# Kernel tuning notes

Measured on AMD Instinct MI355X. Metric: run time of the kernel, lower is better.

The kernel has to match this reference:

```python
import jax, jax.numpy as jnp
import numpy as np

N_NODES = 50000
N_EDGES = 800000
DIM = 256
HEADS = 8
DIM_OUT = 32  # per-head; dim_inner = HEADS*DIM_OUT = 256


def setup_inputs() -> dict:
    key = jax.random.key(0)
    ks = jax.random.split(key, 9)
    s = 1.0 / np.sqrt(DIM)
    inner = HEADS * DIM_OUT
    return {
        "x": jax.random.normal(ks[0], (N_NODES, DIM), dtype=jnp.float32),
        "Wq": jax.random.uniform(ks[1], (DIM, inner), jnp.float32, -s, s),
        "bq": jax.random.uniform(ks[2], (inner,), jnp.float32, -s, s),
        "Wk": jax.random.uniform(ks[3], (DIM, inner), jnp.float32, -s, s),
        "bk": jax.random.uniform(ks[4], (inner,), jnp.float32, -s, s),
        "Wv": jax.random.uniform(ks[5], (DIM, inner), jnp.float32, -s, s),
        "bv": jax.random.uniform(ks[6], (inner,), jnp.float32, -s, s),
        "src": jax.random.randint(ks[7], (N_EDGES,), 0, N_NODES),
        "dst": jax.random.randint(ks[8], (N_EDGES,), 0, N_NODES),
    }


def reference(x, Wq, bq, Wk, bk, Wv, bv, src, dst):
    n = x.shape[0]
    q = (x @ Wq + bq).reshape(n, HEADS, DIM_OUT)
    k = (x @ Wk + bk).reshape(n, HEADS, DIM_OUT)
    v = (x @ Wv + bv).reshape(n, HEADS, DIM_OUT)
    # edge-wise u_dot_v: dot of src query with dst key, per head -> [E, H]
    scores = jnp.einsum('ehd,ehd->eh', q[src], k[dst]) / jnp.sqrt(
        jnp.asarray(DIM_OUT, dtype=x.dtype))
    # segment softmax over incoming edges of each destination node
    m = jax.ops.segment_max(scores, dst, num_segments=n)  # [N, H]
    m = jnp.where(jnp.isfinite(m), m, 0.0)
    e = jnp.exp(scores - m[dst])
    z = jax.ops.segment_sum(e, dst, num_segments=n)  # [N, H]
    p = e / jnp.maximum(z[dst], 1e-16)  # [E, H]
    # u_mul_e_sum: sum over incoming edges of src values weighted by attn
    out = jax.ops.segment_sum(v[src] * p[:, :, None], dst, num_segments=n)
    return out.reshape(n, HEADS * DIM_OUT)  # concat=True
```

## Files before the change

### kernel.cpp

```cpp
#include <hip/hip_runtime.h>
#include <math.h>

#define N_NODES 50000
#define N_EDGES 800000
#define DIM 256
#define HEADS 8
#define DIM_OUT 32
#define INNER 256
#define M_PAD 50048

typedef __attribute__((ext_vector_type(8))) short bf16x8;
typedef __attribute__((ext_vector_type(4))) float f32x4;
typedef __attribute__((ext_vector_type(2))) float f32x2;

__device__ __forceinline__ unsigned short f2bf(float f) {
    unsigned u = __float_as_uint(f);
    unsigned r = (u + 0x7FFFu + ((u >> 16) & 1u)) >> 16;
    return (unsigned short)r;
}

__device__ __forceinline__ f32x2 up2(unsigned u) {
    f32x2 r;
    r.x = __uint_as_float(u << 16);
    r.y = __uint_as_float(u & 0xFFFF0000u);
    return r;
}
__device__ __forceinline__ void up2x4(uint4 r, f32x2* o) {
    o[0] = up2(r.x); o[1] = up2(r.y); o[2] = up2(r.z); o[3] = up2(r.w);
}

__device__ __forceinline__ void gll16(const void* g, void* l) {
    __builtin_amdgcn_global_load_lds(
        (const __attribute__((address_space(1))) unsigned*)(uintptr_t)g,
        (__attribute__((address_space(3))) unsigned*)(unsigned)(uintptr_t)l,
        16, 0, 0);
}

#define NB_CONVX 6256
#define NB_CONVW 768
#define NB_HIST  3125
__global__ __launch_bounds__(256) void prep(
    const float* __restrict__ x,
    const float* __restrict__ Wq, const float* __restrict__ Wk,
    const float* __restrict__ Wv,
    const int* __restrict__ dst,
    unsigned short* __restrict__ xbf, unsigned short* __restrict__ Wt,
    int* __restrict__ deg, int* __restrict__ rank)
{
    int b = blockIdx.x;
    if (b < NB_CONVX) {
        size_t i8 = ((size_t)b * 256 + threadIdx.x) * 8;
        unsigned short h[8];
        if (i8 < (size_t)N_NODES * 256) {
            float4 a = *(const float4*)(x + i8);
            float4 c = *(const float4*)(x + i8 + 4);
            h[0]=f2bf(a.x); h[1]=f2bf(a.y); h[2]=f2bf(a.z); h[3]=f2bf(a.w);
            h[4]=f2bf(c.x); h[5]=f2bf(c.y); h[6]=f2bf(c.z); h[7]=f2bf(c.w);
        } else {
            #pragma unroll
            for (int j = 0; j < 8; j++) h[j] = 0;
        }
        uint4 o;
        o.x = (unsigned)h[0] | ((unsigned)h[1] << 16);
        o.y = (unsigned)h[2] | ((unsigned)h[3] << 16);
        o.z = (unsigned)h[4] | ((unsigned)h[5] << 16);
        o.w = (unsigned)h[6] | ((unsigned)h[7] << 16);
        *(uint4*)(xbf + i8) = o;
    } else if (b < NB_CONVX + NB_CONVW) {
        int idx = (b - NB_CONVX) * 256 + threadIdx.x;
        int z = idx >> 16, r = idx & 65535;
        int k = r >> 8, n = r & 255;
        const float* W = (z == 0) ? Wq : (z == 1) ? Wk : Wv;
        Wt[(size_t)z * 65536 + n * 256 + k] = f2bf(W[k * 256 + n]);
    } else {
        int e = (b - NB_CONVX - NB_CONVW) * 256 + threadIdx.x;
        if (e < N_EDGES) rank[e] = atomicAdd(deg + dst[e], 1);
    }
}

#define GEMM_NWG 1173
__global__ __launch_bounds__(512) void gemm_qkv(
    const unsigned short* __restrict__ xbf,
    const unsigned short* __restrict__ Wt,
    const float* __restrict__ bq, const float* __restrict__ bk,
    const float* __restrict__ bv,
    unsigned short* __restrict__ q, unsigned short* __restrict__ k,
    unsigned short* __restrict__ v,
    const int* __restrict__ deg, int* __restrict__ rowptr)
{
    const int t = threadIdx.x;

    if (blockIdx.x == 0) {
        __shared__ int wsum[8];
        __shared__ int wpre[9];
        int wid = t >> 6, ln = t & 63;
        int carry = 0;
        for (int base = 0; base < N_NODES; base += 2048) {
            int i4 = base + t * 4;
            int4 dv = {0, 0, 0, 0};
            if (i4 < N_NODES) dv = *(const int4*)(deg + i4);
            int sum = dv.x + dv.y + dv.z + dv.w;
            int inc = sum;
            #pragma unroll
            for (int off = 1; off < 64; off <<= 1) {
                int u = __shfl_up(inc, off);
                if (ln >= off) inc += u;
            }
            if (ln == 63) wsum[wid] = inc;
            __syncthreads();
            if (t == 0) {
                int a = 0;
                #pragma unroll
                for (int j = 0; j < 8; j++) { wpre[j] = a; a += wsum[j]; }
                wpre[8] = a;
            }
            __syncthreads();
            if (i4 < N_NODES) {
                int r = carry + wpre[wid] + (inc - sum);
                r += dv.x; rowptr[i4 + 1] = r;
                r += dv.y; rowptr[i4 + 2] = r;
                r += dv.z; rowptr[i4 + 3] = r;
                r += dv.w; rowptr[i4 + 4] = r;
            }
            carry += wpre[8];
            __syncthreads();
        }
        if (t == 0) rowptr[0] = 0;
        return;
    }

    int hw = blockIdx.x - 1;
    int xcd = hw & 7, pos = hw >> 3;
    int lid = (xcd < 5 ? xcd * 147 : 5 * 147 + (xcd - 5) * 146) + pos;
    int panel = lid / 3;
    int z = lid - panel * 3;
    const int row0 = panel * 128;

    const unsigned short* Wz = Wt + (size_t)z * 65536;
    const float* bias = (z == 0) ? bq : (z == 1) ? bk : bv;
    unsigned short* C = (z == 0) ? q : (z == 1) ? k : v;

    __shared__ __align__(16) short As[2][128 * 32];
    __shared__ __align__(16) short Bs[2][256 * 32];

    const int wave = t >> 6;
    const int lane = t & 63;
    const int wm = (wave & 1) * 64;
    const int wn = (wave >> 1) * 64;
    const int lr = lane & 15;
    const int lg = lane >> 4;
    const int srow = lane >> 2;
    const int sch  = lane & 3;

    f32x4 acc[4][4] = {};

#define STAGE(B, K)                                                          \
    do {                                                                     \
        gll16(xbf + (size_t)(row0 + wave * 16 + srow) * 256 + (K) + sch * 8, \
              &As[B][wave * 512]);                                           \
        gll16(Wz + (size_t)(wave * 32 + srow) * 256 + (K) + sch * 8,         \
              &Bs[B][wave * 1024]);                                          \
        gll16(Wz + (size_t)(wave * 32 + 16 + srow) * 256 + (K) + sch * 8,    \
              &Bs[B][wave * 1024 + 512]);                                    \
    } while (0)

    STAGE(0, 0);
    #pragma unroll
    for (int s = 0; s < 8; s++) {
        const int cur = s & 1;
        __syncthreads();
        if (s < 7) STAGE(cur ^ 1, (s + 1) * 32);
        bf16x8 af[4], bfr[4];
        #pragma unroll
        for (int mi = 0; mi < 4; mi++)
            af[mi] = *(const bf16x8*)&As[cur][(wm + mi * 16 + lr) * 32 + lg * 8];
        #pragma unroll
        for (int ni = 0; ni < 4; ni++)
            bfr[ni] = *(const bf16x8*)&Bs[cur][(wn + ni * 16 + lr) * 32 + lg * 8];
        #pragma unroll
        for (int mi = 0; mi < 4; mi++)
            #pragma unroll
            for (int ni = 0; ni < 4; ni++)
                acc[mi][ni] = __builtin_amdgcn_mfma_f32_16x16x32_bf16(
                    af[mi], bfr[ni], acc[mi][ni], 0, 0, 0);
    }
#undef STAGE

    #pragma unroll
    for (int mi = 0; mi < 4; mi++) {
        #pragma unroll
        for (int ni = 0; ni < 4; ni++) {
            int gcol = wn + ni * 16 + lr;
            float bb = bias[gcol];
            #pragma unroll
            for (int r = 0; r < 4; r++) {
                int grow = row0 + wm + mi * 16 + lg * 4 + r;
                if (grow < N_NODES)
                    C[(size_t)grow * 256 + gcol] = f2bf(acc[mi][ni][r] + bb);
            }
        }
    }
}

__global__ __launch_bounds__(256) void csr_scatter(
    const int* __restrict__ src, const int* __restrict__ dst,
    const int* __restrict__ rowptr, const int* __restrict__ rank,
    int* __restrict__ edge_src)
{
    int e = blockIdx.x * 256 + threadIdx.x;
    if (e >= N_EDGES) return;
    edge_src[rowptr[dst[e]] + rank[e]] = src[e];
}

__global__ __launch_bounds__(256) void node_attn(
    const unsigned short* __restrict__ qbf,
    const unsigned short* __restrict__ kbf,
    const unsigned short* __restrict__ vbf,
    const int* __restrict__ rowptr, const int* __restrict__ edge_src,
    float* __restrict__ out)
{
    int node = blockIdx.x * 4 + (threadIdx.x >> 6);
    int lane = threadIdx.x & 63;
    if (node >= N_NODES) return;
    const int half = lane >> 5;
    const int l = lane & 31;

    int beg = rowptr[node], end = rowptr[node + 1];
    int deg = end - beg;

    float* op = out + (size_t)node * 256 + l * 8;
    if (deg <= 0) {
        if (half == 0) {
            float4 z4 = {0.f, 0.f, 0.f, 0.f};
            *(float4*)op = z4;
            *(float4*)(op + 4) = z4;
        }
        return;
    }

    f32x2 kf2[4];
    up2x4(*(const uint4*)(kbf + (size_t)node * 256 + l * 8), kf2);

    const unsigned short* qrow = qbf + l * 8;
    const unsigned short* vrow = vbf + l * 8;

    const float SC = 0.17677669529663687f * 1.4426950408889634f;

    int U = (deg + 1) >> 1;
    U = ((U + 2) / 3) * 3;
    U = __builtin_amdgcn_readfirstlane(U);

    const int i0 = beg + half;
    const int last = end - 1;

    int tmp0 = edge_src[min(i0,     last)];
    int tmp1 = edge_src[min(i0 + 2, last)];
    int idC  = edge_src[min(i0 + 4, last)];
    int idA  = edge_src[min(i0 + 6, last)];
    int idB  = 0;
    uint4 qA = *(const uint4*)(qrow + (size_t)tmp0 * 256);
    uint4 vA = *(const uint4*)(vrow + (size_t)tmp0 * 256);
    uint4 qB = *(const uint4*)(qrow + (size_t)tmp1 * 256);
    uint4 vB = *(const uint4*)(vrow + (size_t)tmp1 * 256);
    uint4 qC, vC;

    float m = -1e30f, zsum = 0.0f;
    f32x2 af2[4] = {};

#define BODY(QW, VW, QL, VL, IDL, IDF, P)                                    \
    do {                                                                     \
        size_t off_ = (size_t)(IDL) * 256;                                   \
        QL = *(const uint4*)(qrow + off_);                                   \
        VL = *(const uint4*)(vrow + off_);                                   \
        int vi_ = i0 + 2 * t + 2 * (P);                                      \
        IDF = edge_src[min(vi_ + 8, last)];                                  \
        f32x2 qf_[4], vf_[4];                                                \
        up2x4(QW, qf_);                                                      \
        up2x4(VW, vf_);                                                      \
        f32x2 d_ = qf_[0] * kf2[0];                                          \
        d_ += qf_[1] * kf2[1];                                               \
        d_ += qf_[2] * kf2[2];                                               \
        d_ += qf_[3] * kf2[3];                                               \
        float s_ = d_.x + d_.y;                                              \
        s_ += __shfl_xor(s_, 1);                                             \
        s_ += __shfl_xor(s_, 2);                                             \
        bool ok_ = vi_ < end;                                                \
        float sc_ = ok_ ? s_ * SC : -1e30f;                                  \
        float mn_ = fmaxf(m, sc_);                                           \
        float w_ = exp2f(sc_ - mn_);                                         \
        w_ = ok_ ? w_ : 0.0f;                                                \
        float al_ = exp2f(m - mn_);                                          \
        zsum = zsum * al_ + w_;                                              \
        f32x2 a2_ = {al_, al_}, w2_ = {w_, w_};                              \
        af2[0] = af2[0] * a2_ + vf_[0] * w2_;                                \
        af2[1] = af2[1] * a2_ + vf_[1] * w2_;                                \
        af2[2] = af2[2] * a2_ + vf_[2] * w2_;                                \
        af2[3] = af2[3] * a2_ + vf_[3] * w2_;                                \
        m = mn_;                                                             \
    } while (0)

    for (int t = 0; t < U; t += 3) {
        BODY(qA, vA, qC, vC, idC, idB, 0);
        BODY(qB, vB, qA, vA, idA, idC, 1);
        BODY(qC, vC, qB, vB, idB, idA, 2);
    }
#undef BODY

    float mo = __shfl_xor(m, 32);
    float mt = fmaxf(m, mo);
    float scale = exp2f(m - mt);
    zsum *= scale;
    zsum += __shfl_xor(zsum, 32);
    #pragma unroll
    for (int j = 0; j < 4; j++) {
        af2[j].x = af2[j].x * scale;
        af2[j].y = af2[j].y * scale;
        af2[j].x += __shfl_xor(af2[j].x, 32);
        af2[j].y += __shfl_xor(af2[j].y, 32);
    }

    float inv = 1.0f / fmaxf(zsum, 1e-16f);
    if (half == 0) {
        float4 o0 = {af2[0].x * inv, af2[0].y * inv, af2[1].x * inv, af2[1].y * inv};
        float4 o1 = {af2[2].x * inv, af2[2].y * inv, af2[3].x * inv, af2[3].y * inv};
        *(float4*)op = o0;
        *(float4*)(op + 4) = o1;
    }
}

extern "C" void kernel_launch(void* const* d_in, const int* in_sizes, int n_in,
                              void* d_out, int out_size, void* d_ws, size_t ws_size,
                              hipStream_t stream) {
    const float* x  = (const float*)d_in[0];
    const float* Wq = (const float*)d_in[1];
    const float* bq = (const float*)d_in[2];
    const float* Wk = (const float*)d_in[3];
    const float* bk = (const float*)d_in[4];
    const float* Wv = (const float*)d_in[5];
    const float* bv = (const float*)d_in[6];
    const int* src  = (const int*)d_in[7];
    const int* dst  = (const int*)d_in[8];
    float* out = (float*)d_out;

    unsigned short* qbf = (unsigned short*)d_ws;
    unsigned short* kbf = qbf + (size_t)N_NODES * INNER;
    unsigned short* vbf = kbf + (size_t)N_NODES * INNER;
    unsigned short* xbf = vbf + (size_t)N_NODES * INNER;
    unsigned short* Wt  = xbf + (size_t)M_PAD * INNER;
    int* deg      = (int*)(Wt + 3 * 65536);
    int* rowptr   = deg + N_NODES;
    int* edge_src = rowptr + (N_NODES + 1);
    int* rank     = edge_src + N_EDGES;

    hipMemsetAsync(deg, 0, (size_t)N_NODES * sizeof(int), stream);

    prep<<<NB_CONVX + NB_CONVW + NB_HIST, 256, 0, stream>>>(
        x, Wq, Wk, Wv, dst, xbf, Wt, deg, rank);

    gemm_qkv<<<GEMM_NWG + 1, 512, 0, stream>>>(
        xbf, Wt, bq, bk, bv, qbf, kbf, vbf, deg, rowptr);

    csr_scatter<<<(N_EDGES + 255) / 256, 256, 0, stream>>>(
        src, dst, rowptr, rank, edge_src);

    node_attn<<<(N_NODES + 3) / 4, 256, 0, stream>>>(
        qbf, kbf, vbf, rowptr, edge_src, out);
}
```

Baseline: 325.4 us.

## Fuse x fp32-to-bf16 conversion into QKV GEMM A-tile staging

Removes the separate pass that converts x to bf16 in the prep kernel. The GEMM now loads fp32 x directly into registers, converts it to bf16, and writes it to LDS, with software prefetch one stage ahead. This drops the intermediate xbf write and re-read of about 25 MB. In exchange, each of the three z-panels reads the fp32 A tile separately, so x is read three times at twice the width, and the A load no longer goes asynchronously through global_load_lds. node_attn is also split into two launches of half the nodes each, which has no clear speed purpose.

```diff
diff --git a/kernel.cpp b/kernel.cpp
--- a/kernel.cpp
+++ b/kernel.cpp
@@ -36,51 +36,31 @@
         16, 0, 0);
 }
 
-#define NB_CONVX 6256
 #define NB_CONVW 768
 #define NB_HIST  3125
 __global__ __launch_bounds__(256) void prep(
-    const float* __restrict__ x,
     const float* __restrict__ Wq, const float* __restrict__ Wk,
     const float* __restrict__ Wv,
     const int* __restrict__ dst,
-    unsigned short* __restrict__ xbf, unsigned short* __restrict__ Wt,
+    unsigned short* __restrict__ Wt,
     int* __restrict__ deg, int* __restrict__ rank)
 {
     int b = blockIdx.x;
-    if (b < NB_CONVX) {
-        size_t i8 = ((size_t)b * 256 + threadIdx.x) * 8;
-        unsigned short h[8];
-        if (i8 < (size_t)N_NODES * 256) {
-            float4 a = *(const float4*)(x + i8);
-            float4 c = *(const float4*)(x + i8 + 4);
-            h[0]=f2bf(a.x); h[1]=f2bf(a.y); h[2]=f2bf(a.z); h[3]=f2bf(a.w);
-            h[4]=f2bf(c.x); h[5]=f2bf(c.y); h[6]=f2bf(c.z); h[7]=f2bf(c.w);
-        } else {
-            #pragma unroll
-            for (int j = 0; j < 8; j++) h[j] = 0;
-        }
-        uint4 o;
-        o.x = (unsigned)h[0] | ((unsigned)h[1] << 16);
-        o.y = (unsigned)h[2] | ((unsigned)h[3] << 16);
-        o.z = (unsigned)h[4] | ((unsigned)h[5] << 16);
-        o.w = (unsigned)h[6] | ((unsigned)h[7] << 16);
-        *(uint4*)(xbf + i8) = o;
-    } else if (b < NB_CONVX + NB_CONVW) {
-        int idx = (b - NB_CONVX) * 256 + threadIdx.x;
+    if (b < NB_CONVW) {
+        int idx = b * 256 + threadIdx.x;
         int z = idx >> 16, r = idx & 65535;
         int k = r >> 8, n = r & 255;
         const float* W = (z == 0) ? Wq : (z == 1) ? Wk : Wv;
         Wt[(size_t)z * 65536 + n * 256 + k] = f2bf(W[k * 256 + n]);
     } else {
-        int e = (b - NB_CONVX - NB_CONVW) * 256 + threadIdx.x;
+        int e = (b - NB_CONVW) * 256 + threadIdx.x;
         if (e < N_EDGES) rank[e] = atomicAdd(deg + dst[e], 1);
     }
 }
 
 #define GEMM_NWG 1173
 __global__ __launch_bounds__(512) void gemm_qkv(
-    const unsigned short* __restrict__ xbf,
+    const float* __restrict__ x,
     const unsigned short* __restrict__ Wt,
     const float* __restrict__ bq, const float* __restrict__ bk,
     const float* __restrict__ bv,
@@ -152,24 +132,52 @@
     const int srow = lane >> 2;
     const int sch  = lane & 3;
 
+    const int arow = row0 + wave * 16 + srow;
+    const bool avalid = arow < N_NODES;
+    const float* aptr = x + (size_t)(avalid ? arow : 0) * 256 + sch * 8;
+    const int aoff = wave * 512 + srow * 32 + sch * 8;
+
     f32x4 acc[4][4] = {};
 
-#define STAGE(B, K)                                                          \
+#define LOADA(RA, RB, K)                                                     \
     do {                                                                     \
-        gll16(xbf + (size_t)(row0 + wave * 16 + srow) * 256 + (K) + sch * 8, \
-              &As[B][wave * 512]);                                           \
+        RA = *(const float4*)(aptr + (K));                                   \
+        RB = *(const float4*)(aptr + (K) + 4);                               \
+        if (!avalid) { RA = {0,0,0,0}; RB = {0,0,0,0}; }                     \
+    } while (0)
+
+#define WRITEA(B, RA, RB)                                                    \
+    do {                                                                     \
+        uint4 o_;                                                            \
+        o_.x = (unsigned)f2bf(RA.x) | ((unsigned)f2bf(RA.y) << 16);          \
+        o_.y = (unsigned)f2bf(RA.z) | ((unsigned)f2bf(RA.w) << 16);         \
+        o_.z = (unsigned)f2bf(RB.x) | ((unsigned)f2bf(RB.y) << 16);         \
+        o_.w = (unsigned)f2bf(RB.z) | ((unsigned)f2bf(RB.w) << 16);         \
+        *(uint4*)&As[B][aoff] = o_;                                          \
+    } while (0)
+
+#define STAGEB(BUF, K)                                                       \
+    do {                                                                     \
         gll16(Wz + (size_t)(wave * 32 + srow) * 256 + (K) + sch * 8,         \
-              &Bs[B][wave * 1024]);                                          \
+              &Bs[BUF][wave * 1024]);                                        \
         gll16(Wz + (size_t)(wave * 32 + 16 + srow) * 256 + (K) + sch * 8,    \
-              &Bs[B][wave * 1024 + 512]);                                    \
+              &Bs[BUF][wave * 1024 + 512]);                                  \
     } while (0)
 
-    STAGE(0, 0);
+    float4 ra, rb;
+    LOADA(ra, rb, 0);
+    STAGEB(0, 0);
+    WRITEA(0, ra, rb);
+
     #pragma unroll
     for (int s = 0; s < 8; s++) {
         const int cur = s & 1;
+        if (s < 7) LOADA(ra, rb, (s + 1) * 32);
         __syncthreads();
-        if (s < 7) STAGE(cur ^ 1, (s + 1) * 32);
+        if (s < 7) {
+            STAGEB(cur ^ 1, (s + 1) * 32);
+            WRITEA(cur ^ 1, ra, rb);
+        }
         bf16x8 af[4], bfr[4];
         #pragma unroll
         for (int mi = 0; mi < 4; mi++)
@@ -184,7 +192,9 @@
                 acc[mi][ni] = __builtin_amdgcn_mfma_f32_16x16x32_bf16(
                     af[mi], bfr[ni], acc[mi][ni], 0, 0, 0);
     }
-#undef STAGE
+#undef LOADA
+#undef WRITEA
+#undef STAGEB
 
     #pragma unroll
     for (int mi = 0; mi < 4; mi++) {
@@ -217,9 +227,9 @@
     const unsigned short* __restrict__ kbf,
     const unsigned short* __restrict__ vbf,
     const int* __restrict__ rowptr, const int* __restrict__ edge_src,
-    float* __restrict__ out)
+    float* __restrict__ out, int node0)
 {
-    int node = blockIdx.x * 4 + (threadIdx.x >> 6);
+    int node = node0 + blockIdx.x * 4 + (threadIdx.x >> 6);
     int lane = threadIdx.x & 63;
     if (node >= N_NODES) return;
     const int half = lane >> 5;
@@ -345,8 +355,7 @@
     unsigned short* qbf = (unsigned short*)d_ws;
     unsigned short* kbf = qbf + (size_t)N_NODES * INNER;
     unsigned short* vbf = kbf + (size_t)N_NODES * INNER;
-    unsigned short* xbf = vbf + (size_t)N_NODES * INNER;
-    unsigned short* Wt  = xbf + (size_t)M_PAD * INNER;
+    unsigned short* Wt  = vbf + (size_t)N_NODES * INNER;
     int* deg      = (int*)(Wt + 3 * 65536);
     int* rowptr   = deg + N_NODES;
     int* edge_src = rowptr + (N_NODES + 1);
@@ -354,15 +363,17 @@
 
     hipMemsetAsync(deg, 0, (size_t)N_NODES * sizeof(int), stream);
 
-    prep<<<NB_CONVX + NB_CONVW + NB_HIST, 256, 0, stream>>>(
-        x, Wq, Wk, Wv, dst, xbf, Wt, deg, rank);
+    prep<<<NB_CONVW + NB_HIST, 256, 0, stream>>>(
+        Wq, Wk, Wv, dst, Wt, deg, rank);
 
     gemm_qkv<<<GEMM_NWG + 1, 512, 0, stream>>>(
-        xbf, Wt, bq, bk, bv, qbf, kbf, vbf, deg, rowptr);
+        x, Wt, bq, bk, bv, qbf, kbf, vbf, deg, rowptr);
 
     csr_scatter<<<(N_EDGES + 255) / 256, 256, 0, stream>>>(
         src, dst, rowptr, rank, edge_src);
 
-    node_attn<<<(N_NODES + 3) / 4, 256, 0, stream>>>(
-        qbf, kbf, vbf, rowptr, edge_src, out);
-}
+    node_attn<<<6250, 256, 0, stream>>>(
+        qbf, kbf, vbf, rowptr, edge_src, out, 0);
+    node_attn<<<6250, 256, 0, stream>>>(
+        qbf, kbf, vbf, rowptr, edge_src, out, 25000);
+}
```

Result: slower. 349.2 us (+7.3%).
